# Kernel tuning notes

Measured on AMD Instinct MI355X. Metric: run time of the kernel, lower is better.

## Reference

```python
import jax, jax.numpy as jnp
import numpy as np

QMIN, QMAX = -128, 127  # 8-bit signed quantized range


def setup_inputs() -> dict:
    key = jax.random.key(0)
    k0, k1, k2, k3 = jax.random.split(key, 4)
    N, Cin, H, W = 64, 128, 56, 56
    Cout, K = 128, 3
    x = jax.random.randint(k0, (N, Cin, H, W), -128, 128, dtype=jnp.int32).astype(jnp.int8)
    weight = jax.random.randint(k1, (Cout, Cin, K, K), -128, 128, dtype=jnp.int32).astype(jnp.int8)
    # int32 bias (already shifted by -Zx*sum(W) in the original quantization flow)
    bias = jax.random.randint(k2, (Cout,), -4096, 4096, dtype=jnp.int32)
    input_scale = jnp.float32(0.02)
    weight_scale = jax.random.uniform(k3, (Cout,), minval=0.001, maxval=0.01, dtype=jnp.float32)  # per-channel
    output_scale = jnp.float32(0.05)
    input_zero_point = -3   # python int, constant
    output_zero_point = -2  # python int, constant
    return {"x": x, "weight": weight, "bias": bias,
            "input_scale": input_scale, "weight_scale": weight_scale,
            "output_scale": output_scale,
            "input_zero_point": input_zero_point,
            "output_zero_point": output_zero_point}


def reference(x, weight, bias, input_scale, weight_scale, output_scale,
              input_zero_point, output_zero_point):
    # pad spatial dims with the INPUT zero point (padding=(1,1), as in the torch module)
    xp = jnp.pad(x, ((0, 0), (0, 0), (1, 1), (1, 1)), constant_values=input_zero_point)
    acc = jax.lax.conv_general_dilated(
        xp.astype(jnp.int32), weight.astype(jnp.int32),
        window_strides=(1, 1), padding='VALID',
        rhs_dilation=(1, 1), dimension_numbers=('NCHW', 'OIHW', 'NCHW'))
    acc = acc + bias[None, :, None, None]                       # [N,Co,Ho,Wo] int32
    # requantize: per-output-channel scale, shift by output zero point
    scale = (input_scale * weight_scale / output_scale)[None, :, None, None]
    out = acc.astype(jnp.float32) * scale + jnp.float32(output_zero_point)
    return jnp.clip(jnp.round(out), QMIN, QMAX).astype(jnp.int8)
```

## Files before the change

kernel.cpp:

```cpp
#include <hip/hip_runtime.h>


#define CIN  128
#define COUT 128
#define HW   56
#define NPIX (HW * HW)
#define ROWS  4
#define QCOLS 58
#define XROW  (QCOLS * CIN)
#define XP_OFF 147456
#define XP_ROWS (64 * QCOLS)

typedef int v4i  __attribute__((ext_vector_type(4)));
typedef int v16i __attribute__((ext_vector_type(16)));

__device__ __forceinline__ void gl16(const void* g, void* l) {
    __builtin_amdgcn_global_load_lds(
        (const __attribute__((address_space(1))) unsigned*)g,
        (__attribute__((address_space(3))) unsigned*)l, 16, 0, 0);
}

__global__ __launch_bounds__(256) void pack_w2(const int* __restrict__ w_g,
                                               unsigned* __restrict__ wp2) {
    int i = blockIdx.x * 256 + threadIdx.x;
    if (i >= 36 * 128 * 8) return;
    int dw   = i & 7;
    int cout = (i >> 3) & 127;
    int step = i >> 10;
    int t  = step >> 2;
    int cb = step & 3;
    unsigned d = 0;
#pragma unroll
    for (int b = 0; b < 4; ++b) {
        int ci = cb * 32 + dw * 4 + b;
        int v = w_g[(cout * CIN + ci) * 9 + t];
        d |= (unsigned)(v & 0xFF) << (8 * b);
    }
    int g  = (cout << 1) | (dw >> 2);
    int gs = g ^ ((g >> 3) & 7);
    wp2[step * 1024 + gs * 4 + (dw & 3)] = d;
}

#define LSTR 57
__global__ __launch_bounds__(256) void repack_x(const int* __restrict__ x_g,
                                                unsigned char* __restrict__ xp,
                                                const int* __restrict__ zp_in_p) {
    __shared__ int lx[CIN * LSTR];
    const int blk = blockIdx.x;
    const int n  = blk / QCOLS;
    const int hp = blk % QCOLS;
    const int tid = threadIdx.x;
    const unsigned zpd = (unsigned)((*zp_in_p) & 0xFF) * 0x01010101u;
    unsigned* row = (unsigned*)(xp + (size_t)blk * XROW);

    if (hp == 0 || hp == QCOLS - 1) {
#pragma unroll
        for (int it = 0; it < 8; ++it) {
            int d = it * 256 + tid;
            if (d < QCOLS * 32) row[d] = zpd;
        }
        return;
    }
    const int h = hp - 1;
    const int* xrow = x_g + (n * CIN * HW + h) * HW;
#pragma unroll
    for (int it = 0; it < 7; ++it) {
        int idx = it * 256 + tid;
        int ci  = idx / 14;
        int w4  = (idx - ci * 14) * 4;
        v4i L = *(const v4i*)(xrow + ci * NPIX + w4);
        int* ld = &lx[ci * LSTR + w4];
        ld[0] = L[0]; ld[1] = L[1]; ld[2] = L[2]; ld[3] = L[3];
    }
    __syncthreads();
#pragma unroll
    for (int it = 0; it < 8; ++it) {
        int d = it * 256 + tid;
        if (d < QCOLS * 32) {
            int wp  = d >> 5;
            int ci4 = d & 31;
            unsigned v = zpd;
            if (wp >= 1 && wp <= HW) {
                const int* lb = &lx[ci4 * 4 * LSTR + (wp - 1)];
                v = (unsigned)(lb[0] & 0xFF) |
                    ((unsigned)(lb[LSTR] & 0xFF) << 8) |
                    ((unsigned)(lb[2 * LSTR] & 0xFF) << 16) |
                    ((unsigned)(lb[3 * LSTR] & 0xFF) << 24);
            }
            row[d] = v;
        }
    }
}

__global__ __launch_bounds__(256, 2) void conv_mfma(
    const unsigned char* __restrict__ xp, const unsigned char* __restrict__ wp2b,
    const int* __restrict__ bias, const float* __restrict__ in_s,
    const float* __restrict__ w_s, const float* __restrict__ out_s,
    const int* __restrict__ zp_out_p, int* __restrict__ out) {
    __shared__ unsigned char xsb[45056];
    __shared__ unsigned char Bb[4][8192];
    __shared__ float scs[COUT];
    __shared__ int   bis[COUT];

    const int n   = blockIdx.x / 14;
    const int ho0 = (blockIdx.x % 14) * ROWS;
    const int tid    = threadIdx.x;
    const int lane   = tid & 63;
    const int wave   = tid >> 6;
    const int lane31 = lane & 31;
    const int hi     = lane >> 5;
    const int hi4    = hi * 4;

    if (tid < COUT) {
        scs[tid] = ((*in_s) / (*out_s)) * w_s[tid];
        bis[tid] = bias[tid];
    }

#define STAGEB(U)                                                             \
    {                                                                         \
        const unsigned char* bs = wp2b + (U) * 8192 + wave * 2048 + lane * 16;\
        unsigned char* bd = &Bb[(U) & 3][wave * 2048];                        \
        gl16(bs, bd);                                                         \
        gl16(bs + 1024, bd + 1024);                                           \
    }

    STAGEB(0); STAGEB(1); STAGEB(2);
    const unsigned char* win = xp + (size_t)(n * QCOLS + ho0) * XROW;
    const int qrel = lane >> 3;
    const int lof  = (qrel * 8 + ((lane & 7) ^ qrel)) * 16;
    for (int i = wave; i < 44; i += 4) {
        int off = i * 1024 + lof;
        if (i == 43 && qrel >= 4) off = 0;
        gl16(win + off, xsb + i * 1024);
    }
    __syncthreads();

    const unsigned* xs = (const unsigned*)xsb;
    int qb0, qb1;
    {
        int px0 = wave * 64 + lane31;
        int px1 = wave * 64 + 32 + lane31;
        if (px1 > ROWS * HW - 1) px1 = ROWS * HW - 1;
        qb0 = (px0 / HW) * QCOLS + (px0 % HW);
        qb1 = (px1 / HW) * QCOLS + (px1 % HW);
    }
    int boff[4];
#pragma unroll
    for (int nt = 0; nt < 4; ++nt) {
        int g = nt * 64 + lane31 * 2 + hi;
        boff[nt] = (g ^ ((g >> 3) & 7)) * 16;
    }

    v16i acc[2][4];
#pragma unroll
    for (int i = 0; i < 2; ++i)
#pragma unroll
        for (int j = 0; j < 4; ++j) acc[i][j] = (v16i)0;

#define COMPUTE(U)                                                            \
    {                                                                         \
        const int t  = (U) >> 1;                                              \
        const int kr = (t * 11) >> 5;                                         \
        const int dq = kr * QCOLS + (t - 3 * kr);                             \
        const int q0 = qb0 + dq, q1 = qb1 + dq;                               \
        const int s0 = (q0 & 7) << 2, s1 = (q1 & 7) << 2;                     \
        const unsigned char* bb = Bb[(U) & 3];                                \
        __builtin_amdgcn_s_setprio(1);                                        \
        _Pragma("unroll")                                                     \
        for (int c = 0; c < 2; ++c) {                                         \
            const int cb = ((U) & 1) * 2 + c;                                 \
            v4i a0 = *(const v4i*)&xs[q0 * 32 + ((cb * 8 + hi4) ^ s0)];       \
            v4i a1 = *(const v4i*)&xs[q1 * 32 + ((cb * 8 + hi4) ^ s1)];       \
            const unsigned char* bc = bb + c * 4096;                          \
            v4i b0 = *(const v4i*)(bc + boff[0]);                             \
            v4i b1 = *(const v4i*)(bc + boff[1]);                             \
            v4i b2 = *(const v4i*)(bc + boff[2]);                             \
            v4i b3 = *(const v4i*)(bc + boff[3]);                             \
            acc[0][0] = __builtin_amdgcn_mfma_i32_32x32x32_i8(b0, a0, acc[0][0], 0, 0, 0); \
            acc[0][1] = __builtin_amdgcn_mfma_i32_32x32x32_i8(b1, a0, acc[0][1], 0, 0, 0); \
            acc[0][2] = __builtin_amdgcn_mfma_i32_32x32x32_i8(b2, a0, acc[0][2], 0, 0, 0); \
            acc[0][3] = __builtin_amdgcn_mfma_i32_32x32x32_i8(b3, a0, acc[0][3], 0, 0, 0); \
            acc[1][0] = __builtin_amdgcn_mfma_i32_32x32x32_i8(b0, a1, acc[1][0], 0, 0, 0); \
            acc[1][1] = __builtin_amdgcn_mfma_i32_32x32x32_i8(b1, a1, acc[1][1], 0, 0, 0); \
            acc[1][2] = __builtin_amdgcn_mfma_i32_32x32x32_i8(b2, a1, acc[1][2], 0, 0, 0); \
            acc[1][3] = __builtin_amdgcn_mfma_i32_32x32x32_i8(b3, a1, acc[1][3], 0, 0, 0); \
        }                                                                     \
        __builtin_amdgcn_s_setprio(0);                                        \
    }

#pragma unroll 1
    for (int u = 0; u < 15; ++u) {
        asm volatile("s_waitcnt vmcnt(4)" ::: "memory");
        __builtin_amdgcn_sched_barrier(0);
        __builtin_amdgcn_s_barrier();
        asm volatile("" ::: "memory");
        STAGEB(u + 3);
        COMPUTE(u);
    }
    asm volatile("s_waitcnt vmcnt(4)" ::: "memory");
    __builtin_amdgcn_sched_barrier(0);
    __builtin_amdgcn_s_barrier();
    COMPUTE(15);
    asm volatile("s_waitcnt vmcnt(2)" ::: "memory");
    __builtin_amdgcn_sched_barrier(0);
    __builtin_amdgcn_s_barrier();
    COMPUTE(16);
    asm volatile("s_waitcnt vmcnt(0)" ::: "memory");
    __builtin_amdgcn_sched_barrier(0);
    __builtin_amdgcn_s_barrier();
    COMPUTE(17);
#undef COMPUTE
#undef STAGEB

    const float zpo = (float)(*zp_out_p);
#pragma unroll
    for (int i = 0; i < 2; ++i) {
        const int px = wave * 64 + i * 32 + lane31;
        if (px < ROWS * HW) {
            int* ob = out + n * COUT * NPIX + ho0 * HW + px;
#pragma unroll
            for (int nt = 0; nt < 4; ++nt) {
#pragma unroll
                for (int reg = 0; reg < 16; ++reg) {
                    int co = nt * 32 + (reg & 3) + 8 * (reg >> 2) + hi4;
                    float f = fmaf((float)(acc[i][nt][reg] + bis[co]), scs[co], zpo);
                    f = rintf(f);
                    f = fminf(fmaxf(f, -128.0f), 127.0f);
                    ob[co * NPIX] = (int)f;
                }
            }
        }
    }
}

extern "C" void kernel_launch(void* const* d_in, const int* in_sizes, int n_in,
                              void* d_out, int out_size, void* d_ws, size_t ws_size,
                              hipStream_t stream) {
    const int* x_g      = (const int*)d_in[0];
    const int* w_g      = (const int*)d_in[1];
    const int* bias     = (const int*)d_in[2];
    const float* in_s   = (const float*)d_in[3];
    const float* w_s    = (const float*)d_in[4];
    const float* out_s  = (const float*)d_in[5];
    const int* zp_in_p  = (const int*)d_in[6];
    const int* zp_out_p = (const int*)d_in[7];
    int* outp = (int*)d_out;
    unsigned* wp2 = (unsigned*)d_ws;
    unsigned char* xpp = (unsigned char*)d_ws + XP_OFF;

    pack_w2<<<(36 * 128 * 8 + 255) / 256, 256, 0, stream>>>(w_g, wp2);
    repack_x<<<XP_ROWS, 256, 0, stream>>>(x_g, xpp, zp_in_p);

    const int nblocks = 64 * (HW / ROWS);
    conv_mfma<<<nblocks, 256, 0, stream>>>(xpp, (const unsigned char*)wp2, bias,
                                           in_s, w_s, out_s, zp_out_p, outp);
}
```

Before: 87.10 us.

## Halve output rows per block and shrink LDS tiles for higher occupancy

```diff
diff --git a/kernel.cpp b/kernel.cpp
--- a/kernel.cpp
+++ b/kernel.cpp
@@ -5,7 +5,7 @@
 #define COUT 128
 #define HW   56
 #define NPIX (HW * HW)
-#define ROWS  4
+#define ROWS  2
 #define QCOLS 58
 #define XROW  (QCOLS * CIN)
 #define XP_OFF 147456
@@ -92,18 +92,18 @@
     }
 }
 
-__global__ __launch_bounds__(256, 2) void conv_mfma(
+__global__ __launch_bounds__(256, 3) void conv_mfma(
     const unsigned char* __restrict__ xp, const unsigned char* __restrict__ wp2b,
     const int* __restrict__ bias, const float* __restrict__ in_s,
     const float* __restrict__ w_s, const float* __restrict__ out_s,
     const int* __restrict__ zp_out_p, int* __restrict__ out) {
-    __shared__ unsigned char xsb[45056];
-    __shared__ unsigned char Bb[4][8192];
+    __shared__ unsigned char xsb[29696];
+    __shared__ unsigned char Bb[4][4096];
     __shared__ float scs[COUT];
     __shared__ int   bis[COUT];
 
-    const int n   = blockIdx.x / 14;
-    const int ho0 = (blockIdx.x % 14) * ROWS;
+    const int n   = blockIdx.x / 28;
+    const int ho0 = (blockIdx.x % 28) * ROWS;
     const int tid    = threadIdx.x;
     const int lane   = tid & 63;
     const int wave   = tid >> 6;
@@ -117,33 +117,20 @@
     }
 
 #define STAGEB(U)                                                             \
-    {                                                                         \
-        const unsigned char* bs = wp2b + (U) * 8192 + wave * 2048 + lane * 16;\
-        unsigned char* bd = &Bb[(U) & 3][wave * 2048];                        \
-        gl16(bs, bd);                                                         \
-        gl16(bs + 1024, bd + 1024);                                           \
-    }
+    gl16(wp2b + (U) * 4096 + tid * 16, &Bb[(U) & 3][wave * 1024]);
 
     STAGEB(0); STAGEB(1); STAGEB(2);
     const unsigned char* win = xp + (size_t)(n * QCOLS + ho0) * XROW;
     const int qrel = lane >> 3;
     const int lof  = (qrel * 8 + ((lane & 7) ^ qrel)) * 16;
-    for (int i = wave; i < 44; i += 4) {
-        int off = i * 1024 + lof;
-        if (i == 43 && qrel >= 4) off = 0;
-        gl16(win + off, xsb + i * 1024);
-    }
+    for (int i = wave; i < 29; i += 4)
+        gl16(win + i * 1024 + lof, xsb + i * 1024);
     __syncthreads();
 
     const unsigned* xs = (const unsigned*)xsb;
-    int qb0, qb1;
-    {
-        int px0 = wave * 64 + lane31;
-        int px1 = wave * 64 + 32 + lane31;
-        if (px1 > ROWS * HW - 1) px1 = ROWS * HW - 1;
-        qb0 = (px0 / HW) * QCOLS + (px0 % HW);
-        qb1 = (px1 / HW) * QCOLS + (px1 % HW);
-    }
+    const int px  = wave * 32 + lane31;
+    const int pxc = px < ROWS * HW ? px : ROWS * HW - 1;
+    const int qb  = (pxc / HW) * QCOLS + (pxc % HW);
     int boff[4];
 #pragma unroll
     for (int nt = 0; nt < 4; ++nt) {
@@ -151,83 +138,68 @@
         boff[nt] = (g ^ ((g >> 3) & 7)) * 16;
     }
 
-    v16i acc[2][4];
-#pragma unroll
-    for (int i = 0; i < 2; ++i)
-#pragma unroll
-        for (int j = 0; j < 4; ++j) acc[i][j] = (v16i)0;
+    v16i acc[4];
+#pragma unroll
+    for (int j = 0; j < 4; ++j) acc[j] = (v16i)0;
 
 #define COMPUTE(U)                                                            \
     {                                                                         \
-        const int t  = (U) >> 1;                                              \
+        const int t  = (U) >> 2;                                              \
         const int kr = (t * 11) >> 5;                                         \
         const int dq = kr * QCOLS + (t - 3 * kr);                             \
-        const int q0 = qb0 + dq, q1 = qb1 + dq;                               \
-        const int s0 = (q0 & 7) << 2, s1 = (q1 & 7) << 2;                     \
+        const int q  = qb + dq;                                               \
+        const int sx = (q & 7) << 2;                                          \
+        const int cb = (U) & 3;                                               \
+        v4i a = *(const v4i*)&xs[q * 32 + ((cb * 8 + hi4) ^ sx)];             \
         const unsigned char* bb = Bb[(U) & 3];                                \
+        v4i b0 = *(const v4i*)(bb + boff[0]);                                 \
+        v4i b1 = *(const v4i*)(bb + boff[1]);                                 \
+        v4i b2 = *(const v4i*)(bb + boff[2]);                                 \
+        v4i b3 = *(const v4i*)(bb + boff[3]);                                 \
         __builtin_amdgcn_s_setprio(1);                                        \
-        _Pragma("unroll")                                                     \
-        for (int c = 0; c < 2; ++c) {                                         \
-            const int cb = ((U) & 1) * 2 + c;                                 \
-            v4i a0 = *(const v4i*)&xs[q0 * 32 + ((cb * 8 + hi4) ^ s0)];       \
-            v4i a1 = *(const v4i*)&xs[q1 * 32 + ((cb * 8 + hi4) ^ s1)];       \
-            const unsigned char* bc = bb + c * 4096;                          \
-            v4i b0 = *(const v4i*)(bc + boff[0]);                             \
-            v4i b1 = *(const v4i*)(bc + boff[1]);                             \
-            v4i b2 = *(const v4i*)(bc + boff[2]);                             \
-            v4i b3 = *(const v4i*)(bc + boff[3]);                             \
-            acc[0][0] = __builtin_amdgcn_mfma_i32_32x32x32_i8(b0, a0, acc[0][0], 0, 0, 0); \
-            acc[0][1] = __builtin_amdgcn_mfma_i32_32x32x32_i8(b1, a0, acc[0][1], 0, 0, 0); \
-            acc[0][2] = __builtin_amdgcn_mfma_i32_32x32x32_i8(b2, a0, acc[0][2], 0, 0, 0); \
-            acc[0][3] = __builtin_amdgcn_mfma_i32_32x32x32_i8(b3, a0, acc[0][3], 0, 0, 0); \
-            acc[1][0] = __builtin_amdgcn_mfma_i32_32x32x32_i8(b0, a1, acc[1][0], 0, 0, 0); \
-            acc[1][1] = __builtin_amdgcn_mfma_i32_32x32x32_i8(b1, a1, acc[1][1], 0, 0, 0); \
-            acc[1][2] = __builtin_amdgcn_mfma_i32_32x32x32_i8(b2, a1, acc[1][2], 0, 0, 0); \
-            acc[1][3] = __builtin_amdgcn_mfma_i32_32x32x32_i8(b3, a1, acc[1][3], 0, 0, 0); \
-        }                                                                     \
+        acc[0] = __builtin_amdgcn_mfma_i32_32x32x32_i8(b0, a, acc[0], 0, 0, 0); \
+        acc[1] = __builtin_amdgcn_mfma_i32_32x32x32_i8(b1, a, acc[1], 0, 0, 0); \
+        acc[2] = __builtin_amdgcn_mfma_i32_32x32x32_i8(b2, a, acc[2], 0, 0, 0); \
+        acc[3] = __builtin_amdgcn_mfma_i32_32x32x32_i8(b3, a, acc[3], 0, 0, 0); \
         __builtin_amdgcn_s_setprio(0);                                        \
     }
 
 #pragma unroll 1
-    for (int u = 0; u < 15; ++u) {
-        asm volatile("s_waitcnt vmcnt(4)" ::: "memory");
+    for (int u = 0; u < 33; ++u) {
+        asm volatile("s_waitcnt vmcnt(2)" ::: "memory");
         __builtin_amdgcn_sched_barrier(0);
         __builtin_amdgcn_s_barrier();
         asm volatile("" ::: "memory");
         STAGEB(u + 3);
         COMPUTE(u);
     }
-    asm volatile("s_waitcnt vmcnt(4)" ::: "memory");
-    __builtin_amdgcn_sched_barrier(0);
-    __builtin_amdgcn_s_barrier();
-    COMPUTE(15);
     asm volatile("s_waitcnt vmcnt(2)" ::: "memory");
     __builtin_amdgcn_sched_barrier(0);
     __builtin_amdgcn_s_barrier();
-    COMPUTE(16);
+    COMPUTE(33);
+    asm volatile("s_waitcnt vmcnt(1)" ::: "memory");
+    __builtin_amdgcn_sched_barrier(0);
+    __builtin_amdgcn_s_barrier();
+    COMPUTE(34);
     asm volatile("s_waitcnt vmcnt(0)" ::: "memory");
     __builtin_amdgcn_sched_barrier(0);
     __builtin_amdgcn_s_barrier();
-    COMPUTE(17);
+    COMPUTE(35);
 #undef COMPUTE
 #undef STAGEB
 
     const float zpo = (float)(*zp_out_p);
-#pragma unroll
-    for (int i = 0; i < 2; ++i) {
-        const int px = wave * 64 + i * 32 + lane31;
-        if (px < ROWS * HW) {
-            int* ob = out + n * COUT * NPIX + ho0 * HW + px;
-#pragma unroll
-            for (int nt = 0; nt < 4; ++nt) {
-#pragma unroll
-                for (int reg = 0; reg < 16; ++reg) {
-                    int co = nt * 32 + (reg & 3) + 8 * (reg >> 2) + hi4;
-                    float f = fmaf((float)(acc[i][nt][reg] + bis[co]), scs[co], zpo);
-                    f = rintf(f);
-                    f = fminf(fmaxf(f, -128.0f), 127.0f);
-                    ob[co * NPIX] = (int)f;
-                }
+    if (px < ROWS * HW) {
+        int* ob = out + n * COUT * NPIX + ho0 * HW + px;
+#pragma unroll
+        for (int nt = 0; nt < 4; ++nt) {
+#pragma unroll
+            for (int reg = 0; reg < 16; ++reg) {
+                int co = nt * 32 + (reg & 3) + 8 * (reg >> 2) + hi4;
+                float f = fmaf((float)(acc[nt][reg] + bis[co]), scs[co], zpo);
+                f = rintf(f);
+                f = fminf(fmaxf(f, -128.0f), 127.0f);
+                ob[co * NPIX] = (int)f;
             }
         }
     }
```

New measurement: 102.8 us. +18.0%, slower.
